# Kernel optimization log

Measured on AMD Instinct MI355X. Metric: run time of the kernel, lower is better.

## Reference

```python
import jax, jax.numpy as jnp
import numpy as np

BSZ, P, D, C = 16, 4096, 256, 512


def setup_inputs() -> dict:
    key = jax.random.key(0)
    k1, k2 = jax.random.split(key)
    x = jax.random.normal(k1, (BSZ, P, D), dtype=jnp.float32)
    kernels = jax.random.normal(k2, (C, D), dtype=jnp.float32) * 0.001
    return {"x": x, "kernels": kernels}


def reference(x, kernels):
    bsz, Pn, d = x.shape
    # (bsz, P, C) projection scores, ReLU'd
    scores = jax.nn.relu(jnp.einsum('bpd,cd->bpc', x, kernels))
    # per-channel argmax over positions -> (bsz, C)
    idx = jnp.argmax(scores, axis=1)
    # scatter_add each kernel row into its winning position
    b_idx = jnp.arange(bsz)[:, None]  # (bsz, 1) broadcast against (bsz, C)
    src = jnp.broadcast_to(kernels, (bsz,) + kernels.shape)  # (bsz, C, d)
    out = jnp.zeros((bsz, Pn, d), dtype=x.dtype).at[b_idx, idx].add(src)
    return out
```

## Files before the change

### kernel.cpp

```cpp
#include <hip/hip_runtime.h>
#include <cstddef>
#include <cstdint>

#define BSZ 16
#define PN  4096
#define DD  256
#define CC  512
#define TP  128
#define TC  128
#define NPT (PN / TP)
#define NKC 8

typedef short bf16x8 __attribute__((ext_vector_type(8)));
typedef float f32x4  __attribute__((ext_vector_type(4)));

#define MEMFENCE() __asm__ __volatile__("" ::: "memory")
#define WAITCNT_VM8 0x1F78
#define WAITCNT_VM0 0x1F70

struct Top2 { float v1, v2; int i1, i2; };

__device__ __forceinline__ void t2_insert(Top2& t, float v, int i) {
  if (v > t.v1 || (v == t.v1 && i < t.i1)) {
    t.v2 = t.v1; t.i2 = t.i1; t.v1 = v; t.i1 = i;
  } else if (v > t.v2 || (v == t.v2 && i < t.i2)) {
    t.v2 = v; t.i2 = i;
  }
}

__device__ __forceinline__ void split4(float4 v, uint2& hp, uint2& lp) {
  uint32_t u0 = __float_as_uint(v.x), u1 = __float_as_uint(v.y),
           u2 = __float_as_uint(v.z), u3 = __float_as_uint(v.w);
  float l0 = v.x - __uint_as_float(u0 & 0xffff0000u);
  float l1 = v.y - __uint_as_float(u1 & 0xffff0000u);
  float l2 = v.z - __uint_as_float(u2 & 0xffff0000u);
  float l3 = v.w - __uint_as_float(u3 & 0xffff0000u);
  hp.x = __builtin_amdgcn_perm(u1, u0, 0x07060302u);
  hp.y = __builtin_amdgcn_perm(u3, u2, 0x07060302u);
  lp.x = __builtin_amdgcn_perm(__float_as_uint(l1), __float_as_uint(l0), 0x07060302u);
  lp.y = __builtin_amdgcn_perm(__float_as_uint(l3), __float_as_uint(l2), 0x07060302u);
}

__device__ __forceinline__ void gld16(const void* gsrc, void* ldst) {
  __builtin_amdgcn_global_load_lds(
      (const __attribute__((address_space(1))) unsigned int*)gsrc,
      (__attribute__((address_space(3))) unsigned int*)ldst, 16, 0, 0);
}

__global__ __launch_bounds__(256) void convert_k_kernel(
    const float* __restrict__ kern, uint32_t* __restrict__ ks) {
  const int kc = blockIdx.x, ct = blockIdx.y;
  const size_t chunk = ((size_t)ct * NKC + kc) * 4096;
#pragma unroll
  for (int s0 = 0; s0 < 2; s0++) {
    int s  = threadIdx.x + s0 * 256;
    int fp = s >> 6, kg = (s >> 4) & 3, lr = s & 15;
    int r  = fp * 16 + lr, k0 = kg * 8;
    const float* src = kern + ((size_t)ct * TC + r) * DD + kc * 32 + k0;
    float4 v0 = *(const float4*)src, v1 = *(const float4*)(src + 4);
    uint2 h0, l0, h1, l1; split4(v0, h0, l0); split4(v1, h1, l1);
    *(uint4*)&ks[chunk + (size_t)s * 4]        = make_uint4(h0.x, h0.y, h1.x, h1.y);
    *(uint4*)&ks[chunk + 2048 + (size_t)s * 4] = make_uint4(l0.x, l0.y, l1.x, l1.y);
  }
}

__global__ __launch_bounds__(256) void score_kernel(
    const float* __restrict__ x, const uint32_t* __restrict__ ks,
    float2* __restrict__ pv2, uint32_t* __restrict__ pix) {

  __shared__ __align__(16) char lds[65536];

  const int ct = blockIdx.x, pt = blockIdx.y, b = blockIdx.z;
  const int tid  = threadIdx.x;
  const int lane = tid & 63, wave = tid >> 6;
  const int wr = wave >> 1, wc = wave & 1;

  const char* xbase = (const char*)(x + ((size_t)b * PN + (size_t)pt * TP) * DD);
  const char* asrc[4];
#pragma unroll
  for (int i = 0; i < 4; i++) {
    int s = i * 256 + tid;
    int swr = s >> 9, sfp = (s >> 7) & 3, sl = (s >> 1) & 63, sh = s & 1;
    int row = swr * 64 + sfp * 16 + (sl & 15);
    asrc[i] = xbase + (size_t)row * (DD * 4) + (sl >> 4) * 32 + sh * 16;
  }
  const char* bsrc = (const char*)ks + ((size_t)ct * NKC) * 16384 + tid * 16;

  f32x4 acc[4][4];
#pragma unroll
  for (int i = 0; i < 4; i++)
#pragma unroll
    for (int j = 0; j < 4; j++) acc[i][j] = (f32x4)0.f;

  auto issue = [&](int kc) {
    char* Ab = lds + (kc & 1) * 16384;
    char* Bb = lds + 32768 + (kc & 1) * 16384;
#pragma unroll
    for (int i = 0; i < 4; i++)
      gld16(asrc[i] + kc * 128, Ab + i * 4096 + tid * 16);
#pragma unroll
    for (int i = 0; i < 4; i++)
      gld16(bsrc + kc * 16384 + i * 4096, Bb + i * 4096 + tid * 16);
  };

  issue(0);
  for (int kc = 0; kc < NKC; kc++) {
    if (kc + 1 < NKC) issue(kc + 1);
    MEMFENCE();
    if (kc + 1 < NKC) {
      __builtin_amdgcn_s_waitcnt(WAITCNT_VM8);
    } else {
      __builtin_amdgcn_s_waitcnt(WAITCNT_VM0);
    }
    __builtin_amdgcn_s_barrier();
    MEMFENCE();

    const char* Ab = lds + (kc & 1) * 16384;
    const char* Bb = lds + 32768 + (kc & 1) * 16384;

    bf16x8 Ah[4], Al[4];
#pragma unroll
    for (int fp = 0; fp < 4; fp++) {
      const float4* ap = (const float4*)(Ab + wr * 8192 + fp * 2048 + lane * 32);
      float4 v0 = ap[0], v1 = ap[1];
      uint2 h0, l0, h1, l1; split4(v0, h0, l0); split4(v1, h1, l1);
      uint4 hh = make_uint4(h0.x, h0.y, h1.x, h1.y);
      uint4 ll = make_uint4(l0.x, l0.y, l1.x, l1.y);
      Ah[fp] = *(bf16x8*)&hh;
      Al[fp] = *(bf16x8*)&ll;
    }
#pragma unroll
    for (int fc = 0; fc < 4; fc++) {
      const char* bp = Bb + wc * 4096 + fc * 1024 + lane * 16;
      bf16x8 Bh = *(const bf16x8*)bp;
      bf16x8 Bl = *(const bf16x8*)(bp + 8192);
#pragma unroll
      for (int fp = 0; fp < 4; fp++) {
        acc[fp][fc] = __builtin_amdgcn_mfma_f32_16x16x32_bf16(Ah[fp], Bh, acc[fp][fc], 0, 0, 0);
        acc[fp][fc] = __builtin_amdgcn_mfma_f32_16x16x32_bf16(Ah[fp], Bl, acc[fp][fc], 0, 0, 0);
        acc[fp][fc] = __builtin_amdgcn_mfma_f32_16x16x32_bf16(Al[fp], Bh, acc[fp][fc], 0, 0, 0);
      }
    }
    MEMFENCE();
    __builtin_amdgcn_s_barrier();
    MEMFENCE();
  }
  __syncthreads();

  const int lr = lane & 15, kg = lane >> 4;
  float4* scratch = (float4*)lds;
  const int slot = wr * 4 + kg;
#pragma unroll
  for (int fc = 0; fc < 4; fc++) {
    Top2 t; t.v1 = -1.f; t.v2 = -1.f; t.i1 = 0x7fffffff; t.i2 = 0x7fffffff;
#pragma unroll
    for (int fp = 0; fp < 4; fp++)
#pragma unroll
      for (int r = 0; r < 4; r++) {
        float v = acc[fp][fc][r]; v = v > 0.f ? v : 0.f;
        t2_insert(t, v, wr * 64 + fp * 16 + kg * 4 + r);
      }
    int c_local = wc * 64 + fc * 16 + lr;
    scratch[slot * TC + c_local] =
        make_float4(t.v1, __int_as_float(t.i1), t.v2, __int_as_float(t.i2));
  }
  __syncthreads();

  if (tid < TC) {
    Top2 t; t.v1 = -1.f; t.v2 = -1.f; t.i1 = 0x7fffffff; t.i2 = 0x7fffffff;
#pragma unroll
    for (int s = 0; s < 8; s++) {
      float4 e = scratch[s * TC + tid];
      t2_insert(t, e.x, __float_as_int(e.y));
      t2_insert(t, e.z, __float_as_int(e.w));
    }
    int c = ct * TC + tid;
    size_t o = ((size_t)b * CC + c) * NPT + pt;
    uint32_t p1 = (uint32_t)(pt * TP + t.i1);
    uint32_t p2 = (uint32_t)(pt * TP + t.i2);
    pv2[o] = make_float2(t.v1, t.v2);
    pix[o] = (p1 << 16) | (p2 & 0xffffu);
  }
}

__global__ __launch_bounds__(64) void reduce_winner_kernel(
    const float2* __restrict__ pv2, const uint32_t* __restrict__ pix,
    const float* __restrict__ x, const float* __restrict__ kern,
    int* __restrict__ winner) {
  const int c = blockIdx.x, b = blockIdx.y;
  const int l = threadIdx.x;

  Top2 t; t.v1 = -1.f; t.v2 = -1.f; t.i1 = 0x7fffffff; t.i2 = 0x7fffffff;
  if (l < NPT) {
    size_t o = ((size_t)b * CC + c) * NPT + l;
    float2 v = pv2[o]; uint32_t ii = pix[o];
    t.v1 = v.x; t.v2 = v.y; t.i1 = (int)(ii >> 16); t.i2 = (int)(ii & 0xffffu);
  }
#pragma unroll
  for (int m = 1; m < 64; m <<= 1) {
    float uv1 = __shfl_xor(t.v1, m, 64);
    int   ui1 = __shfl_xor(t.i1, m, 64);
    float uv2 = __shfl_xor(t.v2, m, 64);
    int   ui2 = __shfl_xor(t.i2, m, 64);
    t2_insert(t, uv1, ui1);
    t2_insert(t, uv2, ui2);
  }

  int win = t.i1;
  if (t.v1 - t.v2 <= 1e-4f * t.v1 + 1e-5f) {
    const float4* x1 = (const float4*)(x + ((size_t)b * PN + t.i1) * DD);
    const float4* x2 = (const float4*)(x + ((size_t)b * PN + t.i2) * DD);
    const float4* kc = (const float4*)(kern + (size_t)c * DD);
    float4 a1 = x1[l], a2 = x2[l], k4 = kc[l];
    float s1 = a1.x * k4.x + a1.y * k4.y + a1.z * k4.z + a1.w * k4.w;
    float s2 = a2.x * k4.x + a2.y * k4.y + a2.z * k4.z + a2.w * k4.w;
#pragma unroll
    for (int m = 1; m < 64; m <<= 1) {
      s1 += __shfl_xor(s1, m, 64);
      s2 += __shfl_xor(s2, m, 64);
    }
    s1 = fmaxf(s1, 0.f); s2 = fmaxf(s2, 0.f);
    if (s2 > s1 || (s2 == s1 && t.i2 < t.i1)) win = t.i2;
  }
  if (l == 0) winner[(size_t)b * CC + c] = win;
}

__global__ __launch_bounds__(256) void write_out_kernel(
    const int* __restrict__ winner, const float* __restrict__ kern,
    float4* __restrict__ out) {
  __shared__ __align__(16) int wrow[CC];
  const int b = blockIdx.y;
  const int tid = threadIdx.x, lane = tid & 63, w = tid >> 6;
  const int p = blockIdx.x * 4 + w;

  *(int2*)&wrow[tid * 2] = *(const int2*)&winner[(size_t)b * CC + tid * 2];
  __syncthreads();

  int4 w0 = *(const int4*)&wrow[lane * 8];
  int4 w1 = *(const int4*)&wrow[lane * 8 + 4];
  int wv[8] = {w0.x, w0.y, w0.z, w0.w, w1.x, w1.y, w1.z, w1.w};

  float4 acc = make_float4(0.f, 0.f, 0.f, 0.f);
#pragma unroll
  for (int j = 0; j < 8; j++) {
    unsigned long long m = __ballot(wv[j] == p);
    while (m) {
      int bit = __ffsll((long long)m) - 1; m &= m - 1;
      int c = bit * 8 + j;
      float4 kv = ((const float4*)(kern + (size_t)c * DD))[lane];
      acc.x += kv.x; acc.y += kv.y; acc.z += kv.z; acc.w += kv.w;
    }
  }
  out[((size_t)b * PN + p) * 64 + lane] = acc;
}

extern "C" void kernel_launch(void* const* d_in, const int* in_sizes, int n_in,
                              void* d_out, int out_size, void* d_ws, size_t ws_size,
                              hipStream_t stream) {
  const float* x    = (const float*)d_in[0];
  const float* kern = (const float*)d_in[1];
  float* out = (float*)d_out;

  char* ws = (char*)d_ws;
  float2*   pv2 = (float2*)ws;
  uint32_t* pix = (uint32_t*)(ws + (size_t)BSZ * CC * NPT * sizeof(float2));
  uint32_t* ks  = (uint32_t*)(ws + 3u * 1024 * 1024);
  int*      win = (int*)(ws + 3u * 1024 * 1024 + 512u * 1024);

  convert_k_kernel<<<dim3(NKC, CC / TC), 256, 0, stream>>>(kern, ks);

  score_kernel<<<dim3(CC / TC, NPT, BSZ), 256, 0, stream>>>(x, ks, pv2, pix);

  reduce_winner_kernel<<<dim3(CC, BSZ), 64, 0, stream>>>(pv2, pix, x, kern, win);

  write_out_kernel<<<dim3(PN / 4, BSZ), 256, 0, stream>>>(win, kern, (float4*)out);
}
```

Baseline: 198.3 us.

## Halve channel tile, swizzle block order, and use single-barrier pipeline in score kernel

Shrinks the score kernel's channel tile from 128 to 64, giving each wave a 32-row by 64-channel slice with fewer accumulators and less LDS. Flattens the grid into a 1D launch with an XCD-aware index remap so neighbouring blocks share x tiles in cache. Reorders the double-buffered loop to wait, barrier once, then prefetch the next stage, which drops the second barrier per iteration. The cost is twice as many blocks, so each x tile is loaded from global memory twice as often, and the loop waits for all loads to finish before it prefetches.

```diff
diff --git a/kernel.cpp b/kernel.cpp
--- a/kernel.cpp
+++ b/kernel.cpp
@@ -7,15 +7,15 @@
 #define DD  256
 #define CC  512
 #define TP  128
-#define TC  128
+#define TC  64
 #define NPT (PN / TP)
+#define NCT (CC / TC)
 #define NKC 8
 
 typedef short bf16x8 __attribute__((ext_vector_type(8)));
 typedef float f32x4  __attribute__((ext_vector_type(4)));
 
 #define MEMFENCE() __asm__ __volatile__("" ::: "memory")
-#define WAITCNT_VM8 0x1F78
 #define WAITCNT_VM0 0x1F70
 
 struct Top2 { float v1, v2; int i1, i2; };
@@ -56,7 +56,7 @@
     int s  = threadIdx.x + s0 * 256;
     int fp = s >> 6, kg = (s >> 4) & 3, lr = s & 15;
     int r  = fp * 16 + lr, k0 = kg * 8;
-    const float* src = kern + ((size_t)ct * TC + r) * DD + kc * 32 + k0;
+    const float* src = kern + ((size_t)ct * 128 + r) * DD + kc * 32 + k0;
     float4 v0 = *(const float4*)src, v1 = *(const float4*)(src + 4);
     uint2 h0, l0, h1, l1; split4(v0, h0, l0); split4(v1, h1, l1);
     *(uint4*)&ks[chunk + (size_t)s * 4]        = make_uint4(h0.x, h0.y, h1.x, h1.y);
@@ -68,61 +68,64 @@
     const float* __restrict__ x, const uint32_t* __restrict__ ks,
     float2* __restrict__ pv2, uint32_t* __restrict__ pix) {
 
-  __shared__ __align__(16) char lds[65536];
-
-  const int ct = blockIdx.x, pt = blockIdx.y, b = blockIdx.z;
-  const int tid  = threadIdx.x;
-  const int lane = tid & 63, wave = tid >> 6;
-  const int wr = wave >> 1, wc = wave & 1;
+  __shared__ __align__(16) char lds[49152];
+
+  const int d  = blockIdx.x;
+  const int L  = (d & 7) * 512 + (d >> 3);
+  const int ct = L & 7;
+  const int pt = (L >> 3) & 31;
+  const int b  = L >> 8;
+
+  const int tid = threadIdx.x;
+  const int lane = tid & 63, w = tid >> 6;
 
   const char* xbase = (const char*)(x + ((size_t)b * PN + (size_t)pt * TP) * DD);
+  const int sfp = (tid >> 7) & 1, sh = (tid >> 6) & 1, sl = tid & 63;
+  const int rowb = sfp * 16 + (sl & 15);
+  const int koff = (sl >> 4) * 32 + sh * 16;
   const char* asrc[4];
 #pragma unroll
-  for (int i = 0; i < 4; i++) {
-    int s = i * 256 + tid;
-    int swr = s >> 9, sfp = (s >> 7) & 3, sl = (s >> 1) & 63, sh = s & 1;
-    int row = swr * 64 + sfp * 16 + (sl & 15);
-    asrc[i] = xbase + (size_t)row * (DD * 4) + (sl >> 4) * 32 + sh * 16;
-  }
-  const char* bsrc = (const char*)ks + ((size_t)ct * NKC) * 16384 + tid * 16;
-
-  f32x4 acc[4][4];
-#pragma unroll
   for (int i = 0; i < 4; i++)
+    asrc[i] = xbase + (size_t)(i * 32 + rowb) * (DD * 4) + koff;
+
+  const char* ksbase = (const char*)ks + (size_t)(ct >> 1) * NKC * 16384 + (ct & 1) * 4096;
+  const char* bsrc[2];
+  bsrc[0] = ksbase + tid * 16;
+  bsrc[1] = ksbase + 8192 + tid * 16;
+
+  f32x4 acc[2][4];
+#pragma unroll
+  for (int i = 0; i < 2; i++)
 #pragma unroll
     for (int j = 0; j < 4; j++) acc[i][j] = (f32x4)0.f;
 
   auto issue = [&](int kc) {
     char* Ab = lds + (kc & 1) * 16384;
-    char* Bb = lds + 32768 + (kc & 1) * 16384;
+    char* Bb = lds + 32768 + (kc & 1) * 8192;
 #pragma unroll
     for (int i = 0; i < 4; i++)
       gld16(asrc[i] + kc * 128, Ab + i * 4096 + tid * 16);
 #pragma unroll
-    for (int i = 0; i < 4; i++)
-      gld16(bsrc + kc * 16384 + i * 4096, Bb + i * 4096 + tid * 16);
+    for (int i = 0; i < 2; i++)
+      gld16(bsrc[i] + kc * 16384, Bb + i * 4096 + tid * 16);
   };
 
   issue(0);
   for (int kc = 0; kc < NKC; kc++) {
-    if (kc + 1 < NKC) issue(kc + 1);
     MEMFENCE();
-    if (kc + 1 < NKC) {
-      __builtin_amdgcn_s_waitcnt(WAITCNT_VM8);
-    } else {
-      __builtin_amdgcn_s_waitcnt(WAITCNT_VM0);
-    }
+    __builtin_amdgcn_s_waitcnt(WAITCNT_VM0);
     __builtin_amdgcn_s_barrier();
     MEMFENCE();
+    if (kc + 1 < NKC) issue(kc + 1);
 
     const char* Ab = lds + (kc & 1) * 16384;
-    const char* Bb = lds + 32768 + (kc & 1) * 16384;
-
-    bf16x8 Ah[4], Al[4];
-#pragma unroll
-    for (int fp = 0; fp < 4; fp++) {
-      const float4* ap = (const float4*)(Ab + wr * 8192 + fp * 2048 + lane * 32);
-      float4 v0 = ap[0], v1 = ap[1];
+    const char* Bb = lds + 32768 + (kc & 1) * 8192;
+
+    bf16x8 Ah[2], Al[2];
+#pragma unroll
+    for (int fp = 0; fp < 2; fp++) {
+      float4 v0 = *(const float4*)(Ab + w * 4096 + fp * 2048 + lane * 16);
+      float4 v1 = *(const float4*)(Ab + w * 4096 + fp * 2048 + 1024 + lane * 16);
       uint2 h0, l0, h1, l1; split4(v0, h0, l0); split4(v1, h1, l1);
       uint4 hh = make_uint4(h0.x, h0.y, h1.x, h1.y);
       uint4 ll = make_uint4(l0.x, l0.y, l1.x, l1.y);
@@ -131,37 +134,32 @@
     }
 #pragma unroll
     for (int fc = 0; fc < 4; fc++) {
-      const char* bp = Bb + wc * 4096 + fc * 1024 + lane * 16;
-      bf16x8 Bh = *(const bf16x8*)bp;
-      bf16x8 Bl = *(const bf16x8*)(bp + 8192);
-#pragma unroll
-      for (int fp = 0; fp < 4; fp++) {
+      bf16x8 Bh = *(const bf16x8*)(Bb + fc * 1024 + lane * 16);
+      bf16x8 Bl = *(const bf16x8*)(Bb + 4096 + fc * 1024 + lane * 16);
+#pragma unroll
+      for (int fp = 0; fp < 2; fp++) {
         acc[fp][fc] = __builtin_amdgcn_mfma_f32_16x16x32_bf16(Ah[fp], Bh, acc[fp][fc], 0, 0, 0);
         acc[fp][fc] = __builtin_amdgcn_mfma_f32_16x16x32_bf16(Ah[fp], Bl, acc[fp][fc], 0, 0, 0);
         acc[fp][fc] = __builtin_amdgcn_mfma_f32_16x16x32_bf16(Al[fp], Bh, acc[fp][fc], 0, 0, 0);
       }
     }
     MEMFENCE();
-    __builtin_amdgcn_s_barrier();
-    MEMFENCE();
-  }
-  __syncthreads();
+  }
 
   const int lr = lane & 15, kg = lane >> 4;
   float4* scratch = (float4*)lds;
-  const int slot = wr * 4 + kg;
+  const int slot = w * 4 + kg;
 #pragma unroll
   for (int fc = 0; fc < 4; fc++) {
     Top2 t; t.v1 = -1.f; t.v2 = -1.f; t.i1 = 0x7fffffff; t.i2 = 0x7fffffff;
 #pragma unroll
-    for (int fp = 0; fp < 4; fp++)
+    for (int fp = 0; fp < 2; fp++)
 #pragma unroll
       for (int r = 0; r < 4; r++) {
         float v = acc[fp][fc][r]; v = v > 0.f ? v : 0.f;
-        t2_insert(t, v, wr * 64 + fp * 16 + kg * 4 + r);
+        t2_insert(t, v, w * 32 + fp * 16 + kg * 4 + r);
       }
-    int c_local = wc * 64 + fc * 16 + lr;
-    scratch[slot * TC + c_local] =
+    scratch[slot * TC + fc * 16 + lr] =
         make_float4(t.v1, __int_as_float(t.i1), t.v2, __int_as_float(t.i2));
   }
   __syncthreads();
@@ -169,7 +167,7 @@
   if (tid < TC) {
     Top2 t; t.v1 = -1.f; t.v2 = -1.f; t.i1 = 0x7fffffff; t.i2 = 0x7fffffff;
 #pragma unroll
-    for (int s = 0; s < 8; s++) {
+    for (int s = 0; s < 16; s++) {
       float4 e = scratch[s * TC + tid];
       t2_insert(t, e.x, __float_as_int(e.y));
       t2_insert(t, e.z, __float_as_int(e.w));
@@ -267,9 +265,9 @@
   uint32_t* ks  = (uint32_t*)(ws + 3u * 1024 * 1024);
   int*      win = (int*)(ws + 3u * 1024 * 1024 + 512u * 1024);
 
-  convert_k_kernel<<<dim3(NKC, CC / TC), 256, 0, stream>>>(kern, ks);
-
-  score_kernel<<<dim3(CC / TC, NPT, BSZ), 256, 0, stream>>>(x, ks, pv2, pix);
+  convert_k_kernel<<<dim3(NKC, CC / 128), 256, 0, stream>>>(kern, ks);
+
+  score_kernel<<<dim3(NCT * NPT * BSZ), 256, 0, stream>>>(x, ks, pv2, pix);
 
   reduce_winner_kernel<<<dim3(CC, BSZ), 64, 0, stream>>>(pv2, pix, x, kern, win);
 
```

New measurement: 209.9 us. 1.06x slower.
